# Optimization experiments

Hardware: AMD Instinct MI355X
Metric: run time of the kernel (lower is better)

The kernel has to match this reference:

```python
import jax, jax.numpy as jnp
import numpy as np

BETA = 0.95
THR = 1.0  # snntorch Leaky default threshold

# Heaviside spike with ATan surrogate gradient (snntorch default, alpha=2):
# d/dx = 1 / (1 + (pi*x)^2)
@jax.custom_vjp
def spike_fn(x):
    return (x > 0).astype(x.dtype)

def _spike_fwd(x):
    return spike_fn(x), x

def _spike_bwd(x, g):
    return (g / (1.0 + (jnp.pi * x) ** 2),)

spike_fn.defvjp(_spike_fwd, _spike_bwd)


def setup_inputs() -> dict:
    key = jax.random.key(0)
    ks = jax.random.split(key, 5)
    T, B, D_in, D_h, D_out = 25, 4096, 784, 1000, 10
    x = jax.random.normal(ks[0], (T, B, D_in), dtype=jnp.float32)
    # Kaiming-uniform-ish init like nn.Linear
    w1 = jax.random.uniform(ks[1], (D_h, D_in), jnp.float32, -1, 1) / np.sqrt(D_in)
    b1 = jax.random.uniform(ks[2], (D_h,), jnp.float32, -1, 1) / np.sqrt(D_in)
    w2 = jax.random.uniform(ks[3], (D_out, D_h), jnp.float32, -1, 1) / np.sqrt(D_h)
    b2 = jax.random.uniform(ks[4], (D_out,), jnp.float32, -1, 1) / np.sqrt(D_h)
    return {"x": x, "w1": w1, "b1": b1, "w2": w2, "b2": b2}


def reference(x, w1, b1, w2, b2):
    B = x.shape[1]
    mem1_0 = jnp.zeros((B, w1.shape[0]), x.dtype)
    mem2_0 = jnp.zeros((B, w2.shape[0]), x.dtype)

    def step(carry, xt):
        mem1, mem2 = carry
        # layer 1: Linear + Leaky (reset-by-subtraction, reset from prior mem)
        cur1 = xt @ w1.T + b1
        reset1 = spike_fn(mem1 - THR)
        mem1 = BETA * mem1 + cur1 - reset1 * THR
        spk1 = spike_fn(mem1 - THR)
        # layer 2
        cur2 = spk1 @ w2.T + b2
        reset2 = spike_fn(mem2 - THR)
        mem2 = BETA * mem2 + cur2 - reset2 * THR
        spk2 = spike_fn(mem2 - THR)
        return (mem1, mem2), spk2

    (mem1, mem2), spk_rec = jax.lax.scan(step, (mem1_0, mem2_0), x)
    return spk_rec, mem2
```

## Files before the change

kernel.cpp:

```cpp
#include <hip/hip_runtime.h>

typedef _Float16 f16;
typedef _Float16 f16x4 __attribute__((ext_vector_type(4)));
typedef _Float16 f16x8 __attribute__((ext_vector_type(8)));
typedef float f32x4 __attribute__((ext_vector_type(4)));

#define T_STEPS 25
#define BATCH   4096
#define DIN     784
#define DH      1000
#define HP      1024
#define DOUT    10
#define MROWS   (T_STEPS * BATCH)
#define KSEG    800
#define KA      (2 * KSEG)
#define KB      (3 * KSEG)
#define WROW    2432
#define NT64    38

__global__ void aconv_kernel(const float* __restrict__ x, f16* __restrict__ Ah)
{
    const int total = MROWS * 200;
    for (int idx = blockIdx.x * blockDim.x + threadIdx.x; idx < total;
         idx += gridDim.x * blockDim.x) {
        const int r  = idx / 200;
        const int c4 = (idx - r * 200) * 4;
        f16x4 hi, lo;
        if (c4 < DIN) {
            const float4 v = *(const float4*)(x + (size_t)r * DIN + c4);
            const float vv[4] = {v.x, v.y, v.z, v.w};
            #pragma unroll
            for (int j = 0; j < 4; ++j) {
                f16 h = (f16)vv[j];
                hi[j] = h;
                lo[j] = (f16)(vv[j] - (float)h);
            }
        } else {
            #pragma unroll
            for (int j = 0; j < 4; ++j) { hi[j] = (f16)0.f; lo[j] = (f16)0.f; }
        }
        *(f16x4*)(Ah + (size_t)r * KA + c4)        = hi;
        *(f16x4*)(Ah + (size_t)r * KA + KSEG + c4) = lo;
    }
}

__global__ void wconv_kernel(const float* __restrict__ w1, const float* __restrict__ b1,
                             const float* __restrict__ w2,
                             f16* __restrict__ Wh, float* __restrict__ b1p,
                             float* __restrict__ w2t)
{
    const int stride = gridDim.x * blockDim.x;
    const int tid0 = blockIdx.x * blockDim.x + threadIdx.x;
    for (int idx = tid0; idx < HP * WROW; idx += stride) {
        const int n  = idx / WROW;
        const int k  = idx - n * WROW;
        f16 v = (f16)0.f;
        if (k < KB) {
            const int seg = k / KSEG;
            const int kc  = k - seg * KSEG;
            float w = (n < DH && kc < DIN) ? w1[n * DIN + kc] : 0.f;
            f16 h = (f16)w;
            v = (seg < 2) ? h : (f16)(w - (float)h);
        }
        Wh[idx] = v;
    }
    for (int idx = tid0; idx < HP; idx += stride)
        b1p[idx] = (idx < DH) ? b1[idx] : 0.f;
    for (int idx = tid0; idx < HP * DOUT; idx += stride) {
        const int h = idx / DOUT;
        const int o = idx - h * DOUT;
        w2t[idx] = (h < DH) ? w2[o * DH + h] : 0.f;
    }
}

#define GL(gp, ldsoff) __builtin_amdgcn_global_load_lds( \
    (const __attribute__((address_space(1))) void*)(gp), \
    (__attribute__((address_space(3))) void*)(lds + (ldsoff)), 16, 0, 0)

#define STAGE64(tt) do { \
    const int _buf = ((tt) & 1) * 8192; \
    const int _ak  = (((tt) < 25) ? (tt) : ((tt) - 25)) * 64; \
    const int _bk  = (tt) * 64; \
    GL(Ag + _ak + 0 * 32 * KA,   _buf + 0 * 2048 + widoff); \
    GL(Ag + _ak + 1 * 32 * KA,   _buf + 1 * 2048 + widoff); \
    GL(Ag + _ak + 2 * 32 * KA,   _buf + 2 * 2048 + widoff); \
    GL(Ag + _ak + 3 * 32 * KA,   _buf + 3 * 2048 + widoff); \
    GL(Bg + _bk + 0 * 32 * WROW, 16384 + _buf + 0 * 2048 + widoff); \
    GL(Bg + _bk + 1 * 32 * WROW, 16384 + _buf + 1 * 2048 + widoff); \
    GL(Bg + _bk + 2 * 32 * WROW, 16384 + _buf + 2 * 2048 + widoff); \
    GL(Bg + _bk + 3 * 32 * WROW, 16384 + _buf + 3 * 2048 + widoff); } while (0)

#define MFMA16(A0, A1, A2, A3, B0, B1, B2, B3) \
    acc[0][0] = __builtin_amdgcn_mfma_f32_16x16x32_f16(A0, B0, acc[0][0], 0, 0, 0); \
    acc[0][1] = __builtin_amdgcn_mfma_f32_16x16x32_f16(A0, B1, acc[0][1], 0, 0, 0); \
    acc[0][2] = __builtin_amdgcn_mfma_f32_16x16x32_f16(A0, B2, acc[0][2], 0, 0, 0); \
    acc[0][3] = __builtin_amdgcn_mfma_f32_16x16x32_f16(A0, B3, acc[0][3], 0, 0, 0); \
    acc[1][0] = __builtin_amdgcn_mfma_f32_16x16x32_f16(A1, B0, acc[1][0], 0, 0, 0); \
    acc[1][1] = __builtin_amdgcn_mfma_f32_16x16x32_f16(A1, B1, acc[1][1], 0, 0, 0); \
    acc[1][2] = __builtin_amdgcn_mfma_f32_16x16x32_f16(A1, B2, acc[1][2], 0, 0, 0); \
    acc[1][3] = __builtin_amdgcn_mfma_f32_16x16x32_f16(A1, B3, acc[1][3], 0, 0, 0); \
    acc[2][0] = __builtin_amdgcn_mfma_f32_16x16x32_f16(A2, B0, acc[2][0], 0, 0, 0); \
    acc[2][1] = __builtin_amdgcn_mfma_f32_16x16x32_f16(A2, B1, acc[2][1], 0, 0, 0); \
    acc[2][2] = __builtin_amdgcn_mfma_f32_16x16x32_f16(A2, B2, acc[2][2], 0, 0, 0); \
    acc[2][3] = __builtin_amdgcn_mfma_f32_16x16x32_f16(A2, B3, acc[2][3], 0, 0, 0); \
    acc[3][0] = __builtin_amdgcn_mfma_f32_16x16x32_f16(A3, B0, acc[3][0], 0, 0, 0); \
    acc[3][1] = __builtin_amdgcn_mfma_f32_16x16x32_f16(A3, B1, acc[3][1], 0, 0, 0); \
    acc[3][2] = __builtin_amdgcn_mfma_f32_16x16x32_f16(A3, B2, acc[3][2], 0, 0, 0); \
    acc[3][3] = __builtin_amdgcn_mfma_f32_16x16x32_f16(A3, B3, acc[3][3], 0, 0, 0);

#define RD(off) (*(const f16x8*)(lds + (off)))
#define LGKM(n) asm volatile("s_waitcnt lgkmcnt(" #n ")" ::: "memory")
#define SB      __builtin_amdgcn_sched_barrier(0)
#define P1      __builtin_amdgcn_s_setprio(1)
#define P0      __builtin_amdgcn_s_setprio(0)

#define BODY64(tt, STG) do { \
    const int bufc = ((tt) & 1) * 8192; \
    f16x8 a00, a01, a02, a03, b00, b01, b02, b03; \
    f16x8 a10, a11, a12, a13, b10, b11, b12, b13; \
    if (STG) STAGE64((tt) + 1); \
    b00 = RD(bbase + bufc + 0 * 1024 + cA0); \
    b01 = RD(bbase + bufc + 1 * 1024 + cA0); \
    b02 = RD(bbase + bufc + 2 * 1024 + cA0); \
    b03 = RD(bbase + bufc + 3 * 1024 + cA0); \
    a00 = RD(abase + bufc + 0 * 1024 + cA0); \
    a01 = RD(abase + bufc + 1 * 1024 + cA0); \
    a02 = RD(abase + bufc + 2 * 1024 + cA0); \
    a03 = RD(abase + bufc + 3 * 1024 + cA0); \
    b10 = RD(bbase + bufc + 0 * 1024 + cA1); \
    b11 = RD(bbase + bufc + 1 * 1024 + cA1); \
    b12 = RD(bbase + bufc + 2 * 1024 + cA1); \
    b13 = RD(bbase + bufc + 3 * 1024 + cA1); \
    a10 = RD(abase + bufc + 0 * 1024 + cA1); \
    a11 = RD(abase + bufc + 1 * 1024 + cA1); \
    a12 = RD(abase + bufc + 2 * 1024 + cA1); \
    a13 = RD(abase + bufc + 3 * 1024 + cA1); \
    LGKM(8); SB;                                   \
    P1; MFMA16(a00, a01, a02, a03, b00, b01, b02, b03) P0; \
    LGKM(0); SB;                                   \
    P1; MFMA16(a10, a11, a12, a13, b10, b11, b12, b13) P0; \
    if (STG) { \
        asm volatile("s_waitcnt vmcnt(0)" ::: "memory"); \
        __builtin_amdgcn_s_barrier(); \
    } \
} while (0)

__global__ __launch_bounds__(256, 2)
void gemm_kernel(const f16* __restrict__ A, const f16* __restrict__ B,
                 const float* __restrict__ bias, float* __restrict__ C)
{
    __shared__ f16 lds[32768];

    const int bid = blockIdx.x;
    const int swz = (bid & 7) * 800 + (bid >> 3);
    const int mt = swz >> 3;
    const int nt = swz & 7;
    const size_t rowBase = (size_t)mt * 128;
    const int colBase = nt * 128;

    const int tid  = threadIdx.x;
    const int wid  = tid >> 6;
    const int lane = tid & 63;
    const int wm = wid >> 1;
    const int wn = wid & 1;

    const int gsw = (tid & 7) ^ ((tid >> 3) & 7);
    const f16* Ag = A + (rowBase + (tid >> 3)) * KA + gsw * 8;
    const f16* Bg = B + (size_t)(colBase + (tid >> 3)) * WROW + gsw * 8;
    const int widoff = wid * 512;

    const int cA0 = (((lane >> 4))     ^ (lane & 7)) * 8;
    const int cA1 = (((lane >> 4) + 4) ^ (lane & 7)) * 8;
    const int abase = (wm * 64 + (lane & 15)) * 64;
    const int bbase = 16384 + (wn * 64 + (lane & 15)) * 64;

    f32x4 acc[4][4];
    #pragma unroll
    for (int m = 0; m < 4; ++m)
        #pragma unroll
        for (int n = 0; n < 4; ++n)
            acc[m][n] = (f32x4){0.f, 0.f, 0.f, 0.f};

    STAGE64(0);
    asm volatile("s_waitcnt vmcnt(0)" ::: "memory");
    __builtin_amdgcn_s_barrier();

    for (int t = 0; t < 36; t += 2) {
        BODY64(t, 1);
        BODY64(t + 1, 1);
    }
    BODY64(36, 1);
    BODY64(37, 0);

    const int c_col0 = colBase + wn * 64 + (lane & 15);
    const size_t c_row0 = rowBase + wm * 64 + (lane >> 4) * 4;
    #pragma unroll
    for (int n = 0; n < 4; ++n) {
        const int gcol = c_col0 + n * 16;
        const float bv = bias[gcol];
        #pragma unroll
        for (int m = 0; m < 4; ++m) {
            const size_t grow = c_row0 + m * 16;
            #pragma unroll
            for (int r = 0; r < 4; ++r)
                C[(grow + r) * HP + gcol] = acc[m][n][r] + bv;
        }
    }
}

__global__ __launch_bounds__(256)
void phase2_kernel(const float* __restrict__ cur1, const float* __restrict__ w2t,
                   const float* __restrict__ b2, float* __restrict__ out)
{
    __shared__ float w2s[HP * DOUT];
    const int tid = threadIdx.x;
    for (int i = tid; i < HP * DOUT; i += 256) w2s[i] = w2t[i];

    const int lane = tid & 63;
    const int wave = tid >> 6;
    const int b = blockIdx.x * 4 + wave;

    float m1[16];
    #pragma unroll
    for (int i = 0; i < 16; ++i) m1[i] = 0.f;
    float m2[DOUT], b2r[DOUT];
    #pragma unroll
    for (int o = 0; o < DOUT; ++o) { m2[o] = 0.f; b2r[o] = b2[o]; }
    __syncthreads();

    for (int t = 0; t < T_STEPS; ++t) {
        const float* cr = cur1 + ((size_t)t * BATCH + b) * HP;
        float p[DOUT];
        #pragma unroll
        for (int o = 0; o < DOUT; ++o) p[o] = 0.f;

        #pragma unroll
        for (int c = 0; c < 4; ++c) {
            const float4 cu = *(const float4*)(cr + c * 256 + lane * 4);
            const float cv[4] = {cu.x, cu.y, cu.z, cu.w};
            #pragma unroll
            for (int j = 0; j < 4; ++j) {
                const float mo = m1[c * 4 + j];
                const float rs = (mo > 1.0f) ? 1.0f : 0.0f;
                const float mn = 0.95f * mo + cv[j] - rs;
                m1[c * 4 + j] = mn;
                if (mn > 1.0f) {
                    const float* wr = w2s + (c * 256 + lane * 4 + j) * DOUT;
                    #pragma unroll
                    for (int o = 0; o < DOUT; ++o) p[o] += wr[o];
                }
            }
        }
        #pragma unroll
        for (int o = 0; o < DOUT; ++o) {
            float v = p[o];
            #pragma unroll
            for (int msk = 32; msk > 0; msk >>= 1) v += __shfl_xor(v, msk, 64);
            p[o] = v;
        }
        #pragma unroll
        for (int o = 0; o < DOUT; ++o) {
            const float cur2 = p[o] + b2r[o];
            const float mo = m2[o];
            const float rs = (mo > 1.0f) ? 1.0f : 0.0f;
            m2[o] = 0.95f * mo + cur2 - rs;
        }
        if (lane < DOUT)
            out[(size_t)t * (BATCH * DOUT) + (size_t)b * DOUT + lane] =
                (m2[lane] > 1.0f) ? 1.0f : 0.0f;
    }
    if (lane < DOUT)
        out[(size_t)T_STEPS * BATCH * DOUT + (size_t)b * DOUT + lane] = m2[lane];
}

extern "C" void kernel_launch(void* const* d_in, const int* in_sizes, int n_in,
                              void* d_out, int out_size, void* d_ws, size_t ws_size,
                              hipStream_t stream)
{
    const float* x  = (const float*)d_in[0];
    const float* w1 = (const float*)d_in[1];
    const float* b1 = (const float*)d_in[2];
    const float* w2 = (const float*)d_in[3];
    const float* b2 = (const float*)d_in[4];
    float* out = (float*)d_out;

    char* wsb = (char*)d_ws;
    f16*   Ah   = (f16*)(wsb);
    f16*   Wh   = (f16*)(wsb + 327680000);
    float* cur1 = (float*)(wsb + 327680000 + 4980736);
    float* b1p  = (float*)(wsb + 327680000 + 4980736 + 419430400);
    float* w2t  = (float*)(wsb + 327680000 + 4980736 + 419430400 + 4096);

    aconv_kernel<<<4096, 256, 0, stream>>>(x, Ah);
    wconv_kernel<<<1024, 256, 0, stream>>>(w1, b1, w2, Wh, b1p, w2t);
    gemm_kernel<<<6400, 256, 0, stream>>>(Ah, Wh, b1p, cur1);
    phase2_kernel<<<1024, 256, 0, stream>>>(cur1, w2t, b2, out);
}
```

Measured before the change: 782.9 us.

## Use 512-thread GEMM blocks with 8 waves and merge prep kernels

The GEMM block grows from 4 to 8 waves in a 2x4 layout. Each wave now computes a 64x32 sub-tile with 8 accumulators instead of 64x64 with 16, and each thread issues 4 global-to-LDS loads per stage instead of 8. The aim is to cut per-wave register pressure, raise the number of resident waves, and spread staging across more threads, at the cost of more LDS reads per MFMA for the A operand. The two conversion kernels are also fused into a single prep launch to save one kernel launch.

```diff
diff --git a/kernel.cpp b/kernel.cpp
--- a/kernel.cpp
+++ b/kernel.cpp
@@ -18,11 +18,16 @@
 #define WROW    2432
 #define NT64    38
 
-__global__ void aconv_kernel(const float* __restrict__ x, f16* __restrict__ Ah)
-{
+__global__ void prep_kernel(const float* __restrict__ x, const float* __restrict__ w1,
+                            const float* __restrict__ b1, const float* __restrict__ w2,
+                            f16* __restrict__ Ah, f16* __restrict__ Wh,
+                            float* __restrict__ b1p, float* __restrict__ w2t)
+{
+    const int stride = gridDim.x * blockDim.x;
+    const int tid0 = blockIdx.x * blockDim.x + threadIdx.x;
+
     const int total = MROWS * 200;
-    for (int idx = blockIdx.x * blockDim.x + threadIdx.x; idx < total;
-         idx += gridDim.x * blockDim.x) {
+    for (int idx = tid0; idx < total; idx += stride) {
         const int r  = idx / 200;
         const int c4 = (idx - r * 200) * 4;
         f16x4 hi, lo;
@@ -42,15 +47,7 @@
         *(f16x4*)(Ah + (size_t)r * KA + c4)        = hi;
         *(f16x4*)(Ah + (size_t)r * KA + KSEG + c4) = lo;
     }
-}
-
-__global__ void wconv_kernel(const float* __restrict__ w1, const float* __restrict__ b1,
-                             const float* __restrict__ w2,
-                             f16* __restrict__ Wh, float* __restrict__ b1p,
-                             float* __restrict__ w2t)
-{
-    const int stride = gridDim.x * blockDim.x;
-    const int tid0 = blockIdx.x * blockDim.x + threadIdx.x;
+
     for (int idx = tid0; idx < HP * WROW; idx += stride) {
         const int n  = idx / WROW;
         const int k  = idx - n * WROW;
@@ -81,32 +78,20 @@
     const int _buf = ((tt) & 1) * 8192; \
     const int _ak  = (((tt) < 25) ? (tt) : ((tt) - 25)) * 64; \
     const int _bk  = (tt) * 64; \
-    GL(Ag + _ak + 0 * 32 * KA,   _buf + 0 * 2048 + widoff); \
-    GL(Ag + _ak + 1 * 32 * KA,   _buf + 1 * 2048 + widoff); \
-    GL(Ag + _ak + 2 * 32 * KA,   _buf + 2 * 2048 + widoff); \
-    GL(Ag + _ak + 3 * 32 * KA,   _buf + 3 * 2048 + widoff); \
-    GL(Bg + _bk + 0 * 32 * WROW, 16384 + _buf + 0 * 2048 + widoff); \
-    GL(Bg + _bk + 1 * 32 * WROW, 16384 + _buf + 1 * 2048 + widoff); \
-    GL(Bg + _bk + 2 * 32 * WROW, 16384 + _buf + 2 * 2048 + widoff); \
-    GL(Bg + _bk + 3 * 32 * WROW, 16384 + _buf + 3 * 2048 + widoff); } while (0)
-
-#define MFMA16(A0, A1, A2, A3, B0, B1, B2, B3) \
+    GL(Ag + _ak + 0 * 64 * KA,   _buf + 0 * 4096 + widoff); \
+    GL(Ag + _ak + 1 * 64 * KA,   _buf + 1 * 4096 + widoff); \
+    GL(Bg + _bk + 0 * 64 * WROW, 16384 + _buf + 0 * 4096 + widoff); \
+    GL(Bg + _bk + 1 * 64 * WROW, 16384 + _buf + 1 * 4096 + widoff); } while (0)
+
+#define MFMA8(A0, A1, A2, A3, B0, B1) \
     acc[0][0] = __builtin_amdgcn_mfma_f32_16x16x32_f16(A0, B0, acc[0][0], 0, 0, 0); \
     acc[0][1] = __builtin_amdgcn_mfma_f32_16x16x32_f16(A0, B1, acc[0][1], 0, 0, 0); \
-    acc[0][2] = __builtin_amdgcn_mfma_f32_16x16x32_f16(A0, B2, acc[0][2], 0, 0, 0); \
-    acc[0][3] = __builtin_amdgcn_mfma_f32_16x16x32_f16(A0, B3, acc[0][3], 0, 0, 0); \
     acc[1][0] = __builtin_amdgcn_mfma_f32_16x16x32_f16(A1, B0, acc[1][0], 0, 0, 0); \
     acc[1][1] = __builtin_amdgcn_mfma_f32_16x16x32_f16(A1, B1, acc[1][1], 0, 0, 0); \
-    acc[1][2] = __builtin_amdgcn_mfma_f32_16x16x32_f16(A1, B2, acc[1][2], 0, 0, 0); \
-    acc[1][3] = __builtin_amdgcn_mfma_f32_16x16x32_f16(A1, B3, acc[1][3], 0, 0, 0); \
     acc[2][0] = __builtin_amdgcn_mfma_f32_16x16x32_f16(A2, B0, acc[2][0], 0, 0, 0); \
     acc[2][1] = __builtin_amdgcn_mfma_f32_16x16x32_f16(A2, B1, acc[2][1], 0, 0, 0); \
-    acc[2][2] = __builtin_amdgcn_mfma_f32_16x16x32_f16(A2, B2, acc[2][2], 0, 0, 0); \
-    acc[2][3] = __builtin_amdgcn_mfma_f32_16x16x32_f16(A2, B3, acc[2][3], 0, 0, 0); \
     acc[3][0] = __builtin_amdgcn_mfma_f32_16x16x32_f16(A3, B0, acc[3][0], 0, 0, 0); \
-    acc[3][1] = __builtin_amdgcn_mfma_f32_16x16x32_f16(A3, B1, acc[3][1], 0, 0, 0); \
-    acc[3][2] = __builtin_amdgcn_mfma_f32_16x16x32_f16(A3, B2, acc[3][2], 0, 0, 0); \
-    acc[3][3] = __builtin_amdgcn_mfma_f32_16x16x32_f16(A3, B3, acc[3][3], 0, 0, 0);
+    acc[3][1] = __builtin_amdgcn_mfma_f32_16x16x32_f16(A3, B1, acc[3][1], 0, 0, 0);
 
 #define RD(off) (*(const f16x8*)(lds + (off)))
 #define LGKM(n) asm volatile("s_waitcnt lgkmcnt(" #n ")" ::: "memory")
@@ -116,36 +101,32 @@
 
 #define BODY64(tt, STG) do { \
     const int bufc = ((tt) & 1) * 8192; \
-    f16x8 a00, a01, a02, a03, b00, b01, b02, b03; \
-    f16x8 a10, a11, a12, a13, b10, b11, b12, b13; \
+    f16x8 a00, a01, a02, a03, b00, b01; \
+    f16x8 a10, a11, a12, a13, b10, b11; \
     if (STG) STAGE64((tt) + 1); \
     b00 = RD(bbase + bufc + 0 * 1024 + cA0); \
     b01 = RD(bbase + bufc + 1 * 1024 + cA0); \
-    b02 = RD(bbase + bufc + 2 * 1024 + cA0); \
-    b03 = RD(bbase + bufc + 3 * 1024 + cA0); \
     a00 = RD(abase + bufc + 0 * 1024 + cA0); \
     a01 = RD(abase + bufc + 1 * 1024 + cA0); \
     a02 = RD(abase + bufc + 2 * 1024 + cA0); \
     a03 = RD(abase + bufc + 3 * 1024 + cA0); \
     b10 = RD(bbase + bufc + 0 * 1024 + cA1); \
     b11 = RD(bbase + bufc + 1 * 1024 + cA1); \
-    b12 = RD(bbase + bufc + 2 * 1024 + cA1); \
-    b13 = RD(bbase + bufc + 3 * 1024 + cA1); \
     a10 = RD(abase + bufc + 0 * 1024 + cA1); \
     a11 = RD(abase + bufc + 1 * 1024 + cA1); \
     a12 = RD(abase + bufc + 2 * 1024 + cA1); \
     a13 = RD(abase + bufc + 3 * 1024 + cA1); \
-    LGKM(8); SB;                                   \
-    P1; MFMA16(a00, a01, a02, a03, b00, b01, b02, b03) P0; \
+    LGKM(6); SB;                                   \
+    P1; MFMA8(a00, a01, a02, a03, b00, b01) P0; \
     LGKM(0); SB;                                   \
-    P1; MFMA16(a10, a11, a12, a13, b10, b11, b12, b13) P0; \
+    P1; MFMA8(a10, a11, a12, a13, b10, b11) P0; \
     if (STG) { \
         asm volatile("s_waitcnt vmcnt(0)" ::: "memory"); \
         __builtin_amdgcn_s_barrier(); \
     } \
 } while (0)
 
-__global__ __launch_bounds__(256, 2)
+__global__ __launch_bounds__(512, 4)
 void gemm_kernel(const f16* __restrict__ A, const f16* __restrict__ B,
                  const float* __restrict__ bias, float* __restrict__ C)
 {
@@ -161,8 +142,8 @@
     const int tid  = threadIdx.x;
     const int wid  = tid >> 6;
     const int lane = tid & 63;
-    const int wm = wid >> 1;
-    const int wn = wid & 1;
+    const int wm = wid >> 2;
+    const int wn = wid & 3;
 
     const int gsw = (tid & 7) ^ ((tid >> 3) & 7);
     const f16* Ag = A + (rowBase + (tid >> 3)) * KA + gsw * 8;
@@ -172,30 +153,27 @@
     const int cA0 = (((lane >> 4))     ^ (lane & 7)) * 8;
     const int cA1 = (((lane >> 4) + 4) ^ (lane & 7)) * 8;
     const int abase = (wm * 64 + (lane & 15)) * 64;
-    const int bbase = 16384 + (wn * 64 + (lane & 15)) * 64;
-
-    f32x4 acc[4][4];
+    const int bbase = 16384 + (wn * 32 + (lane & 15)) * 64;
+
+    f32x4 acc[4][2];
     #pragma unroll
     for (int m = 0; m < 4; ++m)
         #pragma unroll
-        for (int n = 0; n < 4; ++n)
+        for (int n = 0; n < 2; ++n)
             acc[m][n] = (f32x4){0.f, 0.f, 0.f, 0.f};
 
     STAGE64(0);
     asm volatile("s_waitcnt vmcnt(0)" ::: "memory");
     __builtin_amdgcn_s_barrier();
 
-    for (int t = 0; t < 36; t += 2) {
+    for (int t = 0; t < NT64 - 1; ++t)
         BODY64(t, 1);
-        BODY64(t + 1, 1);
-    }
-    BODY64(36, 1);
-    BODY64(37, 0);
-
-    const int c_col0 = colBase + wn * 64 + (lane & 15);
+    BODY64(NT64 - 1, 0);
+
+    const int c_col0 = colBase + wn * 32 + (lane & 15);
     const size_t c_row0 = rowBase + wm * 64 + (lane >> 4) * 4;
     #pragma unroll
-    for (int n = 0; n < 4; ++n) {
+    for (int n = 0; n < 2; ++n) {
         const int gcol = c_col0 + n * 16;
         const float bv = bias[gcol];
         #pragma unroll
@@ -291,8 +269,7 @@
     float* b1p  = (float*)(wsb + 327680000 + 4980736 + 419430400);
     float* w2t  = (float*)(wsb + 327680000 + 4980736 + 419430400 + 4096);
 
-    aconv_kernel<<<4096, 256, 0, stream>>>(x, Ah);
-    wconv_kernel<<<1024, 256, 0, stream>>>(w1, b1, w2, Wh, b1p, w2t);
-    gemm_kernel<<<6400, 256, 0, stream>>>(Ah, Wh, b1p, cur1);
+    prep_kernel<<<4096, 256, 0, stream>>>(x, w1, b1, w2, Ah, Wh, b1p, w2t);
+    gemm_kernel<<<6400, 512, 0, stream>>>(Ah, Wh, b1p, cur1);
     phase2_kernel<<<1024, 256, 0, stream>>>(cur1, w2t, b2, out);
 }
```

After: 805.0 us. +2.8%, slower.
